# Kernel tuning notes

Measured on AMD Instinct MI355X. Metric: run time of the kernel, lower is better.

## Reference

```python
import jax, jax.numpy as jnp
import numpy as np

NUM_HEADS = 16


def setup_inputs() -> dict:
    key = jax.random.key(0)
    k1, k2, k3 = jax.random.split(key, 3)
    S, B, E = 2048, 4, 1024
    std = float(np.sqrt(2.0 / (E + E)))
    query = jax.random.normal(k1, (S, B, E), dtype=jnp.float32)
    in_proj_weight = jax.random.normal(k2, (3 * E, E), dtype=jnp.float32) * std
    in_proj_bias = jnp.zeros((3 * E,), dtype=jnp.float32)
    out_proj_weight = jax.random.normal(k3, (E, E), dtype=jnp.float32) * std
    out_proj_bias = jnp.zeros((E,), dtype=jnp.float32)
    return {
        "query": query,
        "in_proj_weight": in_proj_weight,
        "in_proj_bias": in_proj_bias,
        "out_proj_weight": out_proj_weight,
        "out_proj_bias": out_proj_bias,
    }


def reference(query, in_proj_weight, in_proj_bias, out_proj_weight, out_proj_bias):
    S, B, E = query.shape
    H = NUM_HEADS
    hd = E // H
    scale = hd ** -0.5
    # fused QKV projection: [S, B, 3E]
    lin = jnp.einsum("sbe,fe->sbf", query, in_proj_weight) + in_proj_bias
    # torch layout: view(S, B*H, 3, hd) -> interleaved [h, {q,k,v}, hd]
    lin = lin.reshape(S, B * H, 3, hd)
    q = lin[:, :, 0, :]  # [S, B*H, hd]
    k = lin[:, :, 1, :]
    v = lin[:, :, 2, :]
    # scores: [B*H, S_q, S_k]
    scores = jnp.einsum("sbd,tbd->bst", q, k) * scale
    attn = jax.nn.softmax(scores.astype(jnp.float32), axis=-1).astype(scores.dtype)
    # context: [S, B*H, hd] -> [S, B, E]
    ctx = jnp.einsum("bst,tbd->sbd", attn, v).reshape(S, B, E)
    out = jnp.einsum("sbe,fe->sbf", ctx, out_proj_weight) + out_proj_bias
    return out
```

## Files before the change

kernel.cpp:

```cpp
#include <hip/hip_runtime.h>
#include <hip/hip_bf16.h>

typedef __hip_bfloat16 bf16;
typedef __attribute__((ext_vector_type(8))) short short8;
typedef __attribute__((ext_vector_type(4))) float floatx4;

#define GLD_LDS(g, l) __builtin_amdgcn_global_load_lds( \
    (const __attribute__((address_space(1))) void*)(g), \
    (__attribute__((address_space(3))) void*)(l), 16, 0, 0)

#define CS 0.18033688f

__global__ __launch_bounds__(256)
void cvt3_kernel(const float* __restrict__ q,  bf16* __restrict__ qo,
                 const float* __restrict__ w1, bf16* __restrict__ w1o,
                 const float* __restrict__ w2, bf16* __restrict__ w2o)
{
    const int i = blockIdx.x * 256 + threadIdx.x;
    const float* src; bf16* dst; long off;
    if (i < 1048576)       { src = q;  dst = qo;  off = (long)i * 8; }
    else if (i < 1441792)  { src = w1; dst = w1o; off = (long)(i - 1048576) * 8; }
    else                   { src = w2; dst = w2o; off = (long)(i - 1441792) * 8; }
    floatx4 a = *(const floatx4*)(src + off);
    floatx4 b = *(const floatx4*)(src + off + 4);
    short8 h;
    #pragma unroll
    for (int e = 0; e < 4; ++e) {
        union { bf16 v; short s; } u0, u1;
        u0.v = __float2bfloat16(a[e]); h[e]     = u0.s;
        u1.v = __float2bfloat16(b[e]); h[e + 4] = u1.s;
    }
    *(short8*)(dst + off) = h;
}

__device__ __forceinline__ void stage_f32(const float* __restrict__ src, int ld,
                                          bf16* lds, int t)
{
    const int sr = t >> 1;
    const int sc = (t & 1) * 16;
    const float* g = src + (long)sr * ld + sc;
    floatx4 f[4];
    #pragma unroll
    for (int i = 0; i < 4; ++i) f[i] = *(const floatx4*)(g + i * 4);
    short8 h[2];
    #pragma unroll
    for (int v = 0; v < 2; ++v)
        #pragma unroll
        for (int e = 0; e < 8; ++e) {
            union { bf16 b; short s; } u;
            u.b = __float2bfloat16(f[v * 2 + (e >> 2)][e & 3]);
            h[v][e] = u.s;
        }
    *(short8*)(lds + sr * 32 + sc)     = h[0];
    *(short8*)(lds + sr * 32 + sc + 8) = h[1];
}

template<int EPI, int AF32, int BF32>
__global__ __launch_bounds__(256, 2)
void gemm_bt(const void* __restrict__ Ap, const void* __restrict__ Bp,
             const float* __restrict__ bias,
             void* __restrict__ o0, bf16* __restrict__ o1, bf16* __restrict__ o2,
             int K, int N)
{
    __shared__ __align__(16) bf16 lA[128 * 32];
    __shared__ __align__(16) bf16 lB[128 * 32];

    const int t    = threadIdx.x;
    const int lane = t & 63;
    const int w    = t >> 6;
    const int mBase = blockIdx.y * 128;
    const int nBase = blockIdx.x * 128;
    const int wr = (w >> 1) * 64;
    const int wc = (w & 1) * 64;

    const int rowL = t >> 2;
    const int colL = (t & 3) * 8;
    const bf16* gA0 = (const bf16*)Ap + (long)(mBase + rowL) * K + colL;
    const bf16* gA1 = (const bf16*)Ap + (long)(mBase + rowL + 64) * K + colL;
    const bf16* gB0 = (const bf16*)Bp + (long)(nBase + rowL) * K + colL;
    const bf16* gB1 = (const bf16*)Bp + (long)(nBase + rowL + 64) * K + colL;
    char* lAb = (char*)lA + w * 1024;
    char* lBb = (char*)lB + w * 1024;

    floatx4 acc[4][4] = {};

    for (int k0 = 0; k0 < K; k0 += 32) {
        if constexpr (AF32) {
            stage_f32((const float*)Ap + (long)mBase * K + k0, K, lA, t);
        } else {
            GLD_LDS(gA0 + k0, lAb);
            GLD_LDS(gA1 + k0, lAb + 4096);
        }
        if constexpr (BF32) {
            stage_f32((const float*)Bp + (long)nBase * K + k0, K, lB, t);
        } else {
            GLD_LDS(gB0 + k0, lBb);
            GLD_LDS(gB1 + k0, lBb + 4096);
        }
        asm volatile("s_waitcnt vmcnt(0)" ::: "memory");
        __syncthreads();

        short8 af[4], bfr[4];
        #pragma unroll
        for (int m = 0; m < 4; ++m)
            af[m] = *(const short8*)(lA + (wr + m * 16 + (lane & 15)) * 32 + (lane >> 4) * 8);
        #pragma unroll
        for (int n = 0; n < 4; ++n)
            bfr[n] = *(const short8*)(lB + (wc + n * 16 + (lane & 15)) * 32 + (lane >> 4) * 8);
        #pragma unroll
        for (int m = 0; m < 4; ++m)
            #pragma unroll
            for (int n = 0; n < 4; ++n)
                acc[m][n] = __builtin_amdgcn_mfma_f32_16x16x32_bf16(af[m], bfr[n], acc[m][n], 0, 0, 0);
        __syncthreads();
    }

    #pragma unroll
    for (int m = 0; m < 4; ++m) {
        #pragma unroll
        for (int n = 0; n < 4; ++n) {
            const int col = nBase + wc + n * 16 + (lane & 15);
            const int r0  = mBase + wr + m * 16 + ((lane >> 4) << 2);
            const float bv = bias[col];
            if constexpr (EPI == 0) {
                const int h   = col / 192;
                const int rem = col % 192;
                const int qkv = rem >> 6;
                const int d   = rem & 63;
                #pragma unroll
                for (int j = 0; j < 4; ++j) {
                    const int r = r0 + j;
                    const int s = r >> 2;
                    const int b = r & 3;
                    const float v = acc[m][n][j] + bv;
                    if (qkv == 0)
                        ((bf16*)o0)[(((((b << 4) + h) << 11) + s) << 6) + d] =
                            __float2bfloat16(v * CS);
                    else if (qkv == 1)
                        o1[(((((b << 4) + h) << 11) + s) << 6) + d] = __float2bfloat16(v);
                    else
                        o2[((((b << 4) + h) << 17)) + (d << 11) + s] = __float2bfloat16(v);
                }
            } else {
                #pragma unroll
                for (int j = 0; j < 4; ++j)
                    ((float*)o0)[(long)(r0 + j) * N + col] = acc[m][n][j] + bv;
            }
        }
    }
}

__global__ __launch_bounds__(256, 2)
void attn_kernel(const bf16* __restrict__ Q, const bf16* __restrict__ Kg,
                 const bf16* __restrict__ Vt, bf16* __restrict__ Ctx)
{
    __shared__ __align__(16) bf16 lK[2][64 * 64];
    __shared__ __align__(16) bf16 lV[2][64 * 64];

    const int t    = threadIdx.x;
    const int lane = t & 63;
    const int w    = t >> 6;
    const int f    = lane & 15;
    const int g    = lane >> 4;
    const int bh   = blockIdx.y;
    const int q0   = blockIdx.x * 128 + w * 32;
    const long hb  = (long)bh * 2048 * 64;
    const bf16* Qh = Q  + hb;
    const bf16* Kh = Kg + hb;
    const bf16* Vh = Vt + hb;

    int koff[2], voff[2];
    #pragma unroll
    for (int i = 0; i < 2; ++i) {
        const int X = t * 16 + i * 4096;
        const int r = X >> 7;
        const int c = (X & 127) ^ ((r & 7) << 4);
        const int sr = (r & 3) | ((r & 16) >> 2) | ((r & 12) << 1) | (r & 32);
        koff[i] = sr * 64 + (c >> 1);
        voff[i] = r * 2048 + (c >> 1);
    }

    short8 qf[2][2];
    #pragma unroll
    for (int m = 0; m < 2; ++m)
        #pragma unroll
        for (int kk = 0; kk < 2; ++kk)
            qf[m][kk] = *(const short8*)(Qh + (q0 + m * 16 + f) * 64 + kk * 32 + g * 8);

    short8 ones;
    #pragma unroll
    for (int e = 0; e < 8; ++e) ones[e] = (short)0x3F80;

    floatx4 o[2][4] = {};
    floatx4 dn[2] = {};

    #pragma unroll
    for (int i = 0; i < 2; ++i) {
        GLD_LDS(Kh + koff[i], (char*)lK[0] + w * 1024 + i * 4096);
        GLD_LDS(Vh + voff[i], (char*)lV[0] + w * 1024 + i * 4096);
    }
    asm volatile("s_waitcnt vmcnt(0)" ::: "memory");
    __syncthreads();

    auto tile = [&](const bf16* curK, const bf16* curV,
                    bf16* nxtK, bf16* nxtV, int t0) __attribute__((always_inline)) {
        if (t0 + 64 < 2048) {
            #pragma unroll
            for (int i = 0; i < 2; ++i) {
                GLD_LDS(Kh + (long)(t0 + 64) * 64 + koff[i], (char*)nxtK + w * 1024 + i * 4096);
                GLD_LDS(Vh + voff[i] + (t0 + 64),            (char*)nxtV + w * 1024 + i * 4096);
            }
        }

        short8 kf[4][2];
        #pragma unroll
        for (int n = 0; n < 4; ++n)
            #pragma unroll
            for (int kk = 0; kk < 2; ++kk) {
                const int key = n * 16 + f;
                const int byte = (key * 128 + kk * 64 + g * 16) ^ ((key & 7) << 4);
                kf[n][kk] = *(const short8*)((const char*)curK + byte);
            }

        floatx4 sa2[4][2] = {};
        __builtin_amdgcn_s_setprio(1);
        #pragma unroll
        for (int n = 0; n < 4; ++n)
            #pragma unroll
            for (int m = 0; m < 2; ++m)
                #pragma unroll
                for (int kk = 0; kk < 2; ++kk)
                    sa2[n][m] = __builtin_amdgcn_mfma_f32_16x16x32_bf16(kf[n][kk], qf[m][kk], sa2[n][m], 0, 0, 0);
        __builtin_amdgcn_s_setprio(0);

        short8 vf[4][2];
        #pragma unroll
        for (int n2 = 0; n2 < 4; ++n2)
            #pragma unroll
            for (int kk = 0; kk < 2; ++kk) {
                const int dim = n2 * 16 + f;
                const int byte = (dim * 128 + kk * 64 + g * 16) ^ ((dim & 7) << 4);
                vf[n2][kk] = *(const short8*)((const char*)curV + byte);
            }

        short8 pf[2][2];
        #pragma unroll
        for (int m = 0; m < 2; ++m)
            #pragma unroll
            for (int kk = 0; kk < 2; ++kk)
                #pragma unroll
                for (int e = 0; e < 8; ++e) {
                    union { bf16 b; short s; } u;
                    u.b = __float2bfloat16(exp2f(sa2[2 * kk + (e >> 2)][m][e & 3]));
                    pf[m][kk][e] = u.s;
                }

        __builtin_amdgcn_s_setprio(1);
        #pragma unroll
        for (int m = 0; m < 2; ++m) {
            #pragma unroll
            for (int n2 = 0; n2 < 4; ++n2)
                #pragma unroll
                for (int kk = 0; kk < 2; ++kk)
                    o[m][n2] = __builtin_amdgcn_mfma_f32_16x16x32_bf16(pf[m][kk], vf[n2][kk], o[m][n2], 0, 0, 0);
            #pragma unroll
            for (int kk = 0; kk < 2; ++kk)
                dn[m] = __builtin_amdgcn_mfma_f32_16x16x32_bf16(pf[m][kk], ones, dn[m], 0, 0, 0);
        }
        __builtin_amdgcn_s_setprio(0);

        __syncthreads();
    };

    for (int t0 = 0; t0 < 2048; t0 += 128) {
        tile(lK[0], lV[0], lK[1], lV[1], t0);
        tile(lK[1], lV[1], lK[0], lV[0], t0 + 64);
    }

    const int b = bh >> 4;
    const int h = bh & 15;
    #pragma unroll
    for (int m = 0; m < 2; ++m) {
        float inv[4];
        #pragma unroll
        for (int j = 0; j < 4; ++j)
            inv[j] = 1.f / dn[m][j];
        #pragma unroll
        for (int n2 = 0; n2 < 4; ++n2) {
            const int dim = (h << 6) + n2 * 16 + f;
            #pragma unroll
            for (int j = 0; j < 4; ++j) {
                const int srw = q0 + m * 16 + (g << 2) + j;
                Ctx[(((srw << 2) + b) << 10) + dim] = __float2bfloat16(o[m][n2][j] * inv[j]);
            }
        }
    }
}

extern "C" void kernel_launch(void* const* d_in, const int* in_sizes, int n_in,
                              void* d_out, int out_size, void* d_ws, size_t ws_size,
                              hipStream_t stream)
{
    const float* query = (const float*)d_in[0];
    const float* wIn   = (const float*)d_in[1];
    const float* bIn   = (const float*)d_in[2];
    const float* wOut  = (const float*)d_in[3];
    const float* bOut  = (const float*)d_in[4];

    const size_t HEADSZ = (size_t)64 * 2048 * 64;
    bf16* Qws = (bf16*)d_ws;
    bf16* Kws = Qws + HEADSZ;
    bf16* Vtw = Kws + HEADSZ;
    bf16* Ctx = Vtw + HEADSZ;
    bf16* qbf = Ctx;
    if (ws_size < 4 * HEADSZ * sizeof(bf16)) return;

    const size_t NEED_BIG = (4 * HEADSZ + 3145728 + 1048576) * sizeof(bf16);
    if (ws_size >= NEED_BIG) {
        bf16* wInBf  = Ctx + HEADSZ;
        bf16* wOutBf = wInBf + 3145728;
        cvt3_kernel<<<dim3(6144), 256, 0, stream>>>(query, qbf, wIn, wInBf, wOut, wOutBf);
        gemm_bt<0, 0, 0><<<dim3(24, 64), 256, 0, stream>>>(qbf, wInBf, bIn,
                                                           Qws, Kws, Vtw, 1024, 3072);
        attn_kernel<<<dim3(16, 64), 256, 0, stream>>>(Qws, Kws, Vtw, Ctx);
        gemm_bt<1, 0, 0><<<dim3(8, 64), 256, 0, stream>>>(Ctx, wOutBf, bOut,
                                                          d_out, nullptr, nullptr, 1024, 1024);
    } else {
        cvt3_kernel<<<dim3(4096), 256, 0, stream>>>(query, qbf, nullptr, nullptr, nullptr, nullptr);
        gemm_bt<0, 0, 1><<<dim3(24, 64), 256, 0, stream>>>(qbf, wIn, bIn,
                                                           Qws, Kws, Vtw, 1024, 3072);
        attn_kernel<<<dim3(16, 64), 256, 0, stream>>>(Qws, Kws, Vtw, Ctx);
        gemm_bt<1, 0, 1><<<dim3(8, 64), 256, 0, stream>>>(Ctx, wOut, bOut,
                                                          d_out, nullptr, nullptr, 1024, 1024);
    }
}
```

Baseline: 225.2 us.

## Shrink attention query tile and remap GEMM/attention blocks for XCD-local L2 reuse

The attention kernel now processes 64 queries per block (16 per wave) instead of 128, over a 1D grid of 2048 blocks. The linear block index is decoded so that the eight consecutive blocks the hardware spreads across XCDs take different heads. As a result, the blocks sharing one head's K/V land on the same XCD and can reuse its L2. The GEMM gets a similar XCD-aware swizzle of its block index. The attention change halves the MFMA work per K/V tile held in LDS, so each block's K/V traffic and LDS reads are amortised over fewer queries, in exchange for lower register pressure and more blocks.

Result: no change. 225.9 us (+0.3%).

```diff
diff --git a/kernel.cpp b/kernel.cpp
--- a/kernel.cpp
+++ b/kernel.cpp
@@ -68,8 +68,14 @@
     const int t    = threadIdx.x;
     const int lane = t & 63;
     const int w    = t >> 6;
-    const int mBase = blockIdx.y * 128;
-    const int nBase = blockIdx.x * 128;
+
+    const int nb   = N >> 7;
+    const int lin  = blockIdx.y * nb + blockIdx.x;
+    const int cpx  = (nb << 6) >> 3;
+    const int swz  = (lin & 7) * cpx + (lin >> 3);
+    const int mBase = (swz / nb) * 128;
+    const int nBase = (swz % nb) * 128;
+
     const int wr = (w >> 1) * 64;
     const int wc = (w & 1) * 64;
 
@@ -162,8 +168,9 @@
     const int w    = t >> 6;
     const int f    = lane & 15;
     const int g    = lane >> 4;
-    const int bh   = blockIdx.y;
-    const int q0   = blockIdx.x * 128 + w * 32;
+    const int lin  = blockIdx.x;
+    const int bh   = (lin & 7) | (((lin >> 8) & 7) << 3);
+    const int q0   = ((lin >> 3) & 31) * 64 + w * 16;
     const long hb  = (long)bh * 2048 * 64;
     const bf16* Qh = Q  + hb;
     const bf16* Kh = Kg + hb;
@@ -180,19 +187,17 @@
         voff[i] = r * 2048 + (c >> 1);
     }
 
-    short8 qf[2][2];
-    #pragma unroll
-    for (int m = 0; m < 2; ++m)
-        #pragma unroll
-        for (int kk = 0; kk < 2; ++kk)
-            qf[m][kk] = *(const short8*)(Qh + (q0 + m * 16 + f) * 64 + kk * 32 + g * 8);
+    short8 qf[2];
+    #pragma unroll
+    for (int kk = 0; kk < 2; ++kk)
+        qf[kk] = *(const short8*)(Qh + (q0 + f) * 64 + kk * 32 + g * 8);
 
     short8 ones;
     #pragma unroll
     for (int e = 0; e < 8; ++e) ones[e] = (short)0x3F80;
 
-    floatx4 o[2][4] = {};
-    floatx4 dn[2] = {};
+    floatx4 o[4] = {};
+    floatx4 dn = {};
 
     #pragma unroll
     for (int i = 0; i < 2; ++i) {
@@ -222,15 +227,13 @@
                 kf[n][kk] = *(const short8*)((const char*)curK + byte);
             }
 
-        floatx4 sa2[4][2] = {};
+        floatx4 sa2[4] = {};
         __builtin_amdgcn_s_setprio(1);
         #pragma unroll
         for (int n = 0; n < 4; ++n)
             #pragma unroll
-            for (int m = 0; m < 2; ++m)
-                #pragma unroll
-                for (int kk = 0; kk < 2; ++kk)
-                    sa2[n][m] = __builtin_amdgcn_mfma_f32_16x16x32_bf16(kf[n][kk], qf[m][kk], sa2[n][m], 0, 0, 0);
+            for (int kk = 0; kk < 2; ++kk)
+                sa2[n] = __builtin_amdgcn_mfma_f32_16x16x32_bf16(kf[n][kk], qf[kk], sa2[n], 0, 0, 0);
         __builtin_amdgcn_s_setprio(0);
 
         short8 vf[4][2];
@@ -243,30 +246,25 @@
                 vf[n2][kk] = *(const short8*)((const char*)curV + byte);
             }
 
-        short8 pf[2][2];
-        #pragma unroll
-        for (int m = 0; m < 2; ++m)
+        short8 pf[2];
+        #pragma unroll
+        for (int kk = 0; kk < 2; ++kk)
+            #pragma unroll
+            for (int e = 0; e < 8; ++e) {
+                union { bf16 b; short s; } u;
+                u.b = __float2bfloat16(exp2f(sa2[2 * kk + (e >> 2)][e & 3]));
+                pf[kk][e] = u.s;
+            }
+
+        __builtin_amdgcn_s_setprio(1);
+        #pragma unroll
+        for (int n2 = 0; n2 < 4; ++n2)
             #pragma unroll
             for (int kk = 0; kk < 2; ++kk)
-                #pragma unroll
-                for (int e = 0; e < 8; ++e) {
-                    union { bf16 b; short s; } u;
-                    u.b = __float2bfloat16(exp2f(sa2[2 * kk + (e >> 2)][m][e & 3]));
-                    pf[m][kk][e] = u.s;
-                }
-
-        __builtin_amdgcn_s_setprio(1);
-        #pragma unroll
-        for (int m = 0; m < 2; ++m) {
-            #pragma unroll
-            for (int n2 = 0; n2 < 4; ++n2)
-                #pragma unroll
-                for (int kk = 0; kk < 2; ++kk)
-                    o[m][n2] = __builtin_amdgcn_mfma_f32_16x16x32_bf16(pf[m][kk], vf[n2][kk], o[m][n2], 0, 0, 0);
-            #pragma unroll
-            for (int kk = 0; kk < 2; ++kk)
-                dn[m] = __builtin_amdgcn_mfma_f32_16x16x32_bf16(pf[m][kk], ones, dn[m], 0, 0, 0);
-        }
+                o[n2] = __builtin_amdgcn_mfma_f32_16x16x32_bf16(pf[kk], vf[n2][kk], o[n2], 0, 0, 0);
+        #pragma unroll
+        for (int kk = 0; kk < 2; ++kk)
+            dn = __builtin_amdgcn_mfma_f32_16x16x32_bf16(pf[kk], ones, dn, 0, 0, 0);
         __builtin_amdgcn_s_setprio(0);
 
         __syncthreads();
@@ -279,20 +277,17 @@
 
     const int b = bh >> 4;
     const int h = bh & 15;
-    #pragma unroll
-    for (int m = 0; m < 2; ++m) {
-        float inv[4];
-        #pragma unroll
-        for (int j = 0; j < 4; ++j)
-            inv[j] = 1.f / dn[m][j];
-        #pragma unroll
-        for (int n2 = 0; n2 < 4; ++n2) {
-            const int dim = (h << 6) + n2 * 16 + f;
-            #pragma unroll
-            for (int j = 0; j < 4; ++j) {
-                const int srw = q0 + m * 16 + (g << 2) + j;
-                Ctx[(((srw << 2) + b) << 10) + dim] = __float2bfloat16(o[m][n2][j] * inv[j]);
-            }
+    float inv[4];
+    #pragma unroll
+    for (int j = 0; j < 4; ++j)
+        inv[j] = 1.f / dn[j];
+    #pragma unroll
+    for (int n2 = 0; n2 < 4; ++n2) {
+        const int dim = (h << 6) + n2 * 16 + f;
+        #pragma unroll
+        for (int j = 0; j < 4; ++j) {
+            const int srw = q0 + (g << 2) + j;
+            Ctx[(((srw << 2) + b) << 10) + dim] = __float2bfloat16(o[n2][j] * inv[j]);
         }
     }
 }
@@ -322,14 +317,14 @@
         cvt3_kernel<<<dim3(6144), 256, 0, stream>>>(query, qbf, wIn, wInBf, wOut, wOutBf);
         gemm_bt<0, 0, 0><<<dim3(24, 64), 256, 0, stream>>>(qbf, wInBf, bIn,
                                                            Qws, Kws, Vtw, 1024, 3072);
-        attn_kernel<<<dim3(16, 64), 256, 0, stream>>>(Qws, Kws, Vtw, Ctx);
+        attn_kernel<<<dim3(2048), 256, 0, stream>>>(Qws, Kws, Vtw, Ctx);
         gemm_bt<1, 0, 0><<<dim3(8, 64), 256, 0, stream>>>(Ctx, wOutBf, bOut,
                                                           d_out, nullptr, nullptr, 1024, 1024);
     } else {
         cvt3_kernel<<<dim3(4096), 256, 0, stream>>>(query, qbf, nullptr, nullptr, nullptr, nullptr);
         gemm_bt<0, 0, 1><<<dim3(24, 64), 256, 0, stream>>>(qbf, wIn, bIn,
                                                            Qws, Kws, Vtw, 1024, 3072);
-        attn_kernel<<<dim3(16, 64), 256, 0, stream>>>(Qws, Kws, Vtw, Ctx);
+        attn_kernel<<<dim3(2048), 256, 0, stream>>>(Qws, Kws, Vtw, Ctx);
         gemm_bt<1, 0, 1><<<dim3(8, 64), 256, 0, stream>>>(Ctx, wOut, bOut,
                                                           d_out, nullptr, nullptr, 1024, 1024);
     }
```
